# Performance work log

Hardware: AMD Instinct MI355X
Metric: run time of the kernel (lower is better)

Reference implementation:

```python
import jax, jax.numpy as jnp
import numpy as np

B, H, S, D = 2, 16, 2048, 64
DEGREE = 2
EPS = 1e-4


def setup_inputs() -> dict:
    key = jax.random.key(0)
    kq, kk, kv = jax.random.split(key, 3)
    q = jax.random.normal(kq, (B, H, S, D), dtype=jnp.float32)
    k = jax.random.normal(kk, (B, H, S, D), dtype=jnp.float32)
    v = jax.random.normal(kv, (B, H, S, D), dtype=jnp.float32)
    return {"q": q, "k": k, "v": v}


def reference(q, k, v):
    # dots: [B,H,S,S] = QK^T
    dots = jnp.einsum("bhsd,bhtd->bhst", q, k)
    # polynomial kernel: x^degree, row-normalized with clamped denom
    x = dots ** DEGREE
    denom = jnp.maximum(x.sum(axis=-1, keepdims=True), EPS)
    attn = x / denom
    # weighted V sum: [B,H,S,D]
    return jnp.einsum("bhst,bhtd->bhsd", attn, v)
```

## Files before the change

kernel.cpp:

```cpp
#include <hip/hip_runtime.h>


#define S_LEN 2048
#define DH    64
#define BQ    128
#define BK    64
#define LSTR  72
#define EPSTR 68
#define PSTR  65
#define BH_N  32
#define PER_BH (S_LEN * DH)
#define NT    (S_LEN / BK)

typedef __bf16 bf16x8 __attribute__((ext_vector_type(8)));
typedef __bf16 bf16x2 __attribute__((ext_vector_type(2)));
typedef float  f32x4  __attribute__((ext_vector_type(4)));
typedef float  f32x16 __attribute__((ext_vector_type(16)));
typedef unsigned int uivec2 __attribute__((ext_vector_type(2)));

__device__ __forceinline__ unsigned short f2bf(float f) {
    union { float f; unsigned int u; } x; x.f = f;
    unsigned int u = x.u;
    return (unsigned short)((u + 0x7fffu + ((u >> 16) & 1u)) >> 16);
}

__device__ __forceinline__ unsigned int pack2bf(float lo, float hi) {
#if __has_builtin(__builtin_amdgcn_cvt_pk_bf16_f32)
    bf16x2 p = __builtin_amdgcn_cvt_pk_bf16_f32(lo, hi);
    union { bf16x2 v; unsigned int u; } c; c.v = p;
    return c.u;
#else
    return (unsigned int)f2bf(lo) | ((unsigned int)f2bf(hi) << 16);
#endif
}

__device__ __forceinline__ void pl32swap(unsigned int& a, unsigned int& b) {
#if __has_builtin(__builtin_amdgcn_permlane32_swap)
    uivec2 r = __builtin_amdgcn_permlane32_swap(a, b, false, false);
    a = r[0]; b = r[1];
#else
    asm("v_permlane32_swap_b32 %0, %1" : "+v"(a), "+v"(b));
#endif
}

__global__ __launch_bounds__(256)
void prepass_kernel(const float* __restrict__ kg, const float* __restrict__ vg,
                    unsigned short* __restrict__ kbf, unsigned short* __restrict__ vt)
{
    __shared__ unsigned short Ls[64 * PSTR];
    const int tid = threadIdx.x;
    const int bh  = blockIdx.y;
    const int t0  = blockIdx.x * 64;
    const size_t base = (size_t)bh * PER_BH + (size_t)t0 * DH;

    {
        const float4* src = (const float4*)(kg + base + (size_t)tid * 16);
        float4 a = src[0], b = src[1], c = src[2], d = src[3];
        union { unsigned short h[8]; uint4 v; } u0, u1;
        u0.h[0]=f2bf(a.x); u0.h[1]=f2bf(a.y); u0.h[2]=f2bf(a.z); u0.h[3]=f2bf(a.w);
        u0.h[4]=f2bf(b.x); u0.h[5]=f2bf(b.y); u0.h[6]=f2bf(b.z); u0.h[7]=f2bf(b.w);
        u1.h[0]=f2bf(c.x); u1.h[1]=f2bf(c.y); u1.h[2]=f2bf(c.z); u1.h[3]=f2bf(c.w);
        u1.h[4]=f2bf(d.x); u1.h[5]=f2bf(d.y); u1.h[6]=f2bf(d.z); u1.h[7]=f2bf(d.w);
        uint4* dst = (uint4*)(kbf + base + (size_t)tid * 16);
        dst[0] = u0.v; dst[1] = u1.v;
    }

    const float* vb = vg + base;
    #pragma unroll
    for (int r = 0; r < 4; ++r) {
        int idx = r * 256 + tid;
        int row = idx >> 4, c4 = idx & 15;
        float4 f = ((const float4*)vb)[idx];
        unsigned short* p = &Ls[row * PSTR + c4 * 4];
        p[0] = f2bf(f.x); p[1] = f2bf(f.y); p[2] = f2bf(f.z); p[3] = f2bf(f.w);
    }
    __syncthreads();
    #pragma unroll
    for (int r = 0; r < 2; ++r) {
        int idx = r * 256 + tid;
        int d = idx >> 3, j8 = idx & 7;
        union { unsigned short h[8]; uint4 v; } u;
        #pragma unroll
        for (int jj = 0; jj < 8; ++jj) u.h[jj] = Ls[(j8 * 8 + jj) * PSTR + d];
        *(uint4*)(vt + (size_t)bh * PER_BH + (size_t)d * S_LEN + t0 + j8 * 8) = u.v;
    }
}

__global__ __launch_bounds__(256, 2)
void poly_attn_main(const float* __restrict__ qg,
                    const unsigned short* __restrict__ kbf,
                    const unsigned short* __restrict__ vtbf,
                    float* __restrict__ og)
{
    __shared__ __align__(16) unsigned short smem[4 * 64 * LSTR];
    #define KS_BASE(b)  ((b) * 64 * LSTR)
    #define VTS_BASE(b) ((2 + (b)) * 64 * LSTR)

    const int tid  = threadIdx.x;
    const int lane = tid & 63;
    const int w    = tid >> 6;
    const int l31  = lane & 31;
    const int h    = lane >> 5;

    const int bh = blockIdx.y;
    const int q0 = blockIdx.x * BQ;

    const float* qb = qg + ((size_t)bh * S_LEN + q0) * DH;
    const unsigned short* kb  = kbf  + (size_t)bh * PER_BH;
    const unsigned short* vtb = vtbf + (size_t)bh * PER_BH;
    float* ob = og + ((size_t)bh * S_LEN + q0) * DH;

    bf16x8 qfrag[4];
    #pragma unroll
    for (int ks = 0; ks < 4; ++ks) {
        const float* qp = qb + (32 * w + l31) * DH + ks * 16 + h * 8;
        float4 f0 = *(const float4*)qp;
        float4 f1 = *(const float4*)(qp + 4);
        union { unsigned int d[4]; bf16x8 v; } u;
        u.d[0] = pack2bf(f0.x, f0.y);
        u.d[1] = pack2bf(f0.z, f0.w);
        u.d[2] = pack2bf(f1.x, f1.y);
        u.d[3] = pack2bf(f1.z, f1.w);
        qfrag[ks] = u.v;
    }

    f32x16 oacc[2];
    #pragma unroll
    for (int mt = 0; mt < 2; ++mt)
        #pragma unroll
        for (int r = 0; r < 16; ++r) oacc[mt][r] = 0.f;
    float dsum = 0.f;

    const int srow = tid >> 3;
    const int sc8  = tid & 7;

    uint4 kreg[2], vreg[2];
    #pragma unroll
    for (int it = 0; it < 2; ++it) {
        int row = srow + it * 32;
        kreg[it] = *(const uint4*)(kb + (size_t)row * DH + sc8 * 8);
        vreg[it] = *(const uint4*)(vtb + (size_t)row * S_LEN + sc8 * 8);
    }
    #pragma unroll
    for (int it = 0; it < 2; ++it) {
        int row = srow + it * 32;
        *(uint4*)&smem[KS_BASE(0)  + row * LSTR + sc8 * 8] = kreg[it];
        *(uint4*)&smem[VTS_BASE(0) + row * LSTR + sc8 * 8] = vreg[it];
    }
    __syncthreads();

    for (int t = 0; t < NT; ++t) {
        const int cur = t & 1;
        if (t + 1 < NT) {
            const int t0n = (t + 1) * BK;
            #pragma unroll
            for (int it = 0; it < 2; ++it) {
                int row = srow + it * 32;
                kreg[it] = *(const uint4*)(kb + (size_t)(t0n + row) * DH + sc8 * 8);
                vreg[it] = *(const uint4*)(vtb + (size_t)row * S_LEN + t0n + sc8 * 8);
            }
        }

        unsigned int bfrag[4][4];
        #pragma unroll
        for (int jt = 0; jt < 2; ++jt) {
            f32x16 acc;
            #pragma unroll
            for (int r = 0; r < 16; ++r) acc[r] = 0.f;
            #pragma unroll
            for (int ks = 0; ks < 4; ++ks) {
                bf16x8 kf = *(const bf16x8*)&smem[KS_BASE(cur) + (jt * 32 + l31) * LSTR + ks * 16 + h * 8];
                acc = __builtin_amdgcn_mfma_f32_32x32x16_bf16(kf, qfrag[ks], acc, 0, 0, 0);
            }
            unsigned int pk[4][2];
            #pragma unroll
            for (int g = 0; g < 4; ++g) {
                float x0 = acc[4*g+0], x1 = acc[4*g+1], x2 = acc[4*g+2], x3 = acc[4*g+3];
                x0 *= x0; x1 *= x1; x2 *= x2; x3 *= x3;
                dsum += (x0 + x1) + (x2 + x3);
                pk[g][0] = pack2bf(x0, x1);
                pk[g][1] = pack2bf(x2, x3);
            }
            #pragma unroll
            for (int e = 0; e < 2; ++e) {
                unsigned int a0 = pk[2*e][0], b0 = pk[2*e+1][0];
                unsigned int a1 = pk[2*e][1], b1 = pk[2*e+1][1];
                pl32swap(a0, b0);
                pl32swap(a1, b1);
                const int ks = jt * 2 + e;
                bfrag[ks][0] = a0; bfrag[ks][1] = a1;
                bfrag[ks][2] = b0; bfrag[ks][3] = b1;
            }
        }

        #pragma unroll
        for (int mt = 0; mt < 2; ++mt) {
            #pragma unroll
            for (int ks = 0; ks < 4; ++ks) {
                bf16x8 vf = *(const bf16x8*)&smem[VTS_BASE(cur) + (mt * 32 + l31) * LSTR + ks * 16 + h * 8];
                union { unsigned int d[4]; bf16x8 v; } u;
                u.d[0] = bfrag[ks][0]; u.d[1] = bfrag[ks][1];
                u.d[2] = bfrag[ks][2]; u.d[3] = bfrag[ks][3];
                oacc[mt] = __builtin_amdgcn_mfma_f32_32x32x16_bf16(vf, u.v, oacc[mt], 0, 0, 0);
            }
        }

        if (t + 1 < NT) {
            #pragma unroll
            for (int it = 0; it < 2; ++it) {
                int row = srow + it * 32;
                *(uint4*)&smem[KS_BASE(cur ^ 1)  + row * LSTR + sc8 * 8] = kreg[it];
                *(uint4*)&smem[VTS_BASE(cur ^ 1) + row * LSTR + sc8 * 8] = vreg[it];
            }
            __syncthreads();
        }
    }

    float tot = dsum + __shfl_xor(dsum, 32);
    float inv = 1.0f / fmaxf(tot, 1e-4f);

    __syncthreads();
    float* ep = (float*)smem + (size_t)w * (32 * EPSTR);
    #pragma unroll
    for (int mt = 0; mt < 2; ++mt) {
        #pragma unroll
        for (int g = 0; g < 4; ++g) {
            f32x4 vv;
            vv[0] = oacc[mt][4*g+0] * inv;
            vv[1] = oacc[mt][4*g+1] * inv;
            vv[2] = oacc[mt][4*g+2] * inv;
            vv[3] = oacc[mt][4*g+3] * inv;
            *(f32x4*)&ep[l31 * EPSTR + mt * 32 + 8 * g + 4 * h] = vv;
        }
    }
    const int quad4 = lane >> 4;
    const int c4    = lane & 15;
    #pragma unroll
    for (int rr = 0; rr < 8; ++rr) {
        int row = rr * 4 + quad4;
        f32x4 vv = *(const f32x4*)&ep[row * EPSTR + c4 * 4];
        *(f32x4*)&ob[(32 * w + row) * DH + c4 * 4] = vv;
    }
    #undef KS_BASE
    #undef VTS_BASE
}

__global__ __launch_bounds__(256, 2)
void poly_attn_fallback(const float* __restrict__ qg, const float* __restrict__ kg,
                        const float* __restrict__ vg, float* __restrict__ og)
{
    __shared__ unsigned short Qs[64 * LSTR];
    __shared__ unsigned short Ksl[64 * LSTR];
    __shared__ unsigned short Vt[64 * LSTR];
    __shared__ unsigned short Xsl[64 * LSTR];

    const int tid  = threadIdx.x;
    const int lane = tid & 63;
    const int w    = tid >> 6;
    const int c    = lane & 15;
    const int quad = lane >> 4;
    const int i0   = w * 16;

    const int bh = blockIdx.y;
    const int q0 = blockIdx.x * 64;

    const float* qb = qg + ((size_t)bh * S_LEN + q0) * DH;
    const float* kb = kg + (size_t)bh * S_LEN * DH;
    const float* vb = vg + (size_t)bh * S_LEN * DH;
    float*       ob = og + ((size_t)bh * S_LEN + q0) * DH;

    {
        const float4* qf4 = (const float4*)qb;
        #pragma unroll
        for (int r = 0; r < 4; ++r) {
            int idx = r * 256 + tid;
            int row = idx >> 4, c4 = idx & 15;
            float4 f = qf4[idx];
            ushort4 hh;
            hh.x = f2bf(f.x); hh.y = f2bf(f.y); hh.z = f2bf(f.z); hh.w = f2bf(f.w);
            *(ushort4*)&Qs[row * LSTR + c4 * 4] = hh;
        }
    }

    f32x4 oacc[4];
    #pragma unroll
    for (int t = 0; t < 4; ++t) { oacc[t][0]=0.f; oacc[t][1]=0.f; oacc[t][2]=0.f; oacc[t][3]=0.f; }
    float dsum[4] = {0.f, 0.f, 0.f, 0.f};

    for (int t0 = 0; t0 < S_LEN; t0 += 64) {
        __syncthreads();
        {
            const float4* kf4 = (const float4*)(kb + (size_t)t0 * DH);
            const float4* vf4 = (const float4*)(vb + (size_t)t0 * DH);
            #pragma unroll
            for (int r = 0; r < 4; ++r) {
                int idx = r * 256 + tid;
                int row = idx >> 4, c4 = idx & 15;
                float4 f = kf4[idx];
                ushort4 hh;
                hh.x = f2bf(f.x); hh.y = f2bf(f.y); hh.z = f2bf(f.z); hh.w = f2bf(f.w);
                *(ushort4*)&Ksl[row * LSTR + c4 * 4] = hh;
                float4 g = vf4[idx];
                int d0 = c4 * 4;
                Vt[(d0 + 0) * LSTR + row] = f2bf(g.x);
                Vt[(d0 + 1) * LSTR + row] = f2bf(g.y);
                Vt[(d0 + 2) * LSTR + row] = f2bf(g.z);
                Vt[(d0 + 3) * LSTR + row] = f2bf(g.w);
            }
        }
        __syncthreads();

        f32x4 xacc[4];
        #pragma unroll
        for (int t = 0; t < 4; ++t) { xacc[t][0]=0.f; xacc[t][1]=0.f; xacc[t][2]=0.f; xacc[t][3]=0.f; }
        #pragma unroll
        for (int k0 = 0; k0 < 64; k0 += 32) {
            bf16x8 af = *(const bf16x8*)&Qs[(i0 + c) * LSTR + k0 + quad * 8];
            #pragma unroll
            for (int tn = 0; tn < 4; ++tn) {
                bf16x8 bfg = *(const bf16x8*)&Ksl[(tn * 16 + c) * LSTR + k0 + quad * 8];
                xacc[tn] = __builtin_amdgcn_mfma_f32_16x16x32_bf16(af, bfg, xacc[tn], 0, 0, 0);
            }
        }
        #pragma unroll
        for (int tn = 0; tn < 4; ++tn)
            #pragma unroll
            for (int r = 0; r < 4; ++r) {
                float xv = xacc[tn][r];
                float xs = xv * xv;
                dsum[r] += xs;
                Xsl[(i0 + quad * 4 + r) * LSTR + tn * 16 + c] = f2bf(xs);
            }
        __syncthreads();

        #pragma unroll
        for (int k0 = 0; k0 < 64; k0 += 32) {
            bf16x8 af = *(const bf16x8*)&Xsl[(i0 + c) * LSTR + k0 + quad * 8];
            #pragma unroll
            for (int tn = 0; tn < 4; ++tn) {
                bf16x8 bfg = *(const bf16x8*)&Vt[(tn * 16 + c) * LSTR + k0 + quad * 8];
                oacc[tn] = __builtin_amdgcn_mfma_f32_16x16x32_bf16(af, bfg, oacc[tn], 0, 0, 0);
            }
        }
    }

    #pragma unroll
    for (int r = 0; r < 4; ++r) {
        float s = dsum[r];
        s += __shfl_xor(s, 1);
        s += __shfl_xor(s, 2);
        s += __shfl_xor(s, 4);
        s += __shfl_xor(s, 8);
        dsum[r] = 1.0f / fmaxf(s, 1e-4f);
    }
    #pragma unroll
    for (int tn = 0; tn < 4; ++tn)
        #pragma unroll
        for (int r = 0; r < 4; ++r)
            ob[(i0 + quad * 4 + r) * DH + tn * 16 + c] = oacc[tn][r] * dsum[r];
}

extern "C" void kernel_launch(void* const* d_in, const int* in_sizes, int n_in,
                              void* d_out, int out_size, void* d_ws, size_t ws_size,
                              hipStream_t stream) {
    (void)in_sizes; (void)n_in; (void)out_size;
    const float* q = (const float*)d_in[0];
    const float* k = (const float*)d_in[1];
    const float* v = (const float*)d_in[2];
    float* o = (float*)d_out;

    const size_t elems = (size_t)BH_N * PER_BH;
    const size_t need  = 2 * elems * sizeof(unsigned short);

    if (ws_size >= need) {
        unsigned short* kbf = (unsigned short*)d_ws;
        unsigned short* vtb = kbf + elems;
        prepass_kernel<<<dim3(S_LEN / 64, BH_N), 256, 0, stream>>>(k, v, kbf, vtb);
        poly_attn_main<<<dim3(S_LEN / BQ, BH_N), 256, 0, stream>>>(q, kbf, vtb, o);
    } else {
        poly_attn_fallback<<<dim3(S_LEN / 64, BH_N), 256, 0, stream>>>(q, k, v, o);
    }
}
```

Measured before the change: 159.2 us.

## Halve query tile and split key block across wave pairs with smem reduction

Query tile per block drops from 128 to 64 rows, and each pair of waves now shares 32 query rows, with each wave handling half of every 64-key tile. Partial outputs and row denominators are combined through shared memory in the epilogue. Launch bounds are raised to 4 blocks per SM. This doubles the grid and cuts per-wave MFMA work per tile to improve occupancy and latency hiding, at the cost of twice the K/V tile loads per query and an extra cross-wave reduction.

```diff
diff --git a/kernel.cpp b/kernel.cpp
--- a/kernel.cpp
+++ b/kernel.cpp
@@ -3,7 +3,7 @@
 
 #define S_LEN 2048
 #define DH    64
-#define BQ    128
+#define BQ    64
 #define BK    64
 #define LSTR  72
 #define EPSTR 68
@@ -86,19 +86,22 @@
     }
 }
 
-__global__ __launch_bounds__(256, 2)
+__global__ __launch_bounds__(256, 4)
 void poly_attn_main(const float* __restrict__ qg,
                     const unsigned short* __restrict__ kbf,
                     const unsigned short* __restrict__ vtbf,
                     float* __restrict__ og)
 {
     __shared__ __align__(16) unsigned short smem[4 * 64 * LSTR];
+    __shared__ float dbuf[128];
     #define KS_BASE(b)  ((b) * 64 * LSTR)
     #define VTS_BASE(b) ((2 + (b)) * 64 * LSTR)
 
     const int tid  = threadIdx.x;
     const int lane = tid & 63;
     const int w    = tid >> 6;
+    const int p    = w >> 1;
+    const int e    = w & 1;
     const int l31  = lane & 31;
     const int h    = lane >> 5;
 
@@ -113,7 +116,7 @@
     bf16x8 qfrag[4];
     #pragma unroll
     for (int ks = 0; ks < 4; ++ks) {
-        const float* qp = qb + (32 * w + l31) * DH + ks * 16 + h * 8;
+        const float* qp = qb + (32 * p + l31) * DH + ks * 16 + h * 8;
         float4 f0 = *(const float4*)qp;
         float4 f1 = *(const float4*)(qp + 4);
         union { unsigned int d[4]; bf16x8 v; } u;
@@ -161,46 +164,43 @@
             }
         }
 
-        unsigned int bfrag[4][4];
-        #pragma unroll
-        for (int jt = 0; jt < 2; ++jt) {
-            f32x16 acc;
-            #pragma unroll
-            for (int r = 0; r < 16; ++r) acc[r] = 0.f;
-            #pragma unroll
-            for (int ks = 0; ks < 4; ++ks) {
-                bf16x8 kf = *(const bf16x8*)&smem[KS_BASE(cur) + (jt * 32 + l31) * LSTR + ks * 16 + h * 8];
-                acc = __builtin_amdgcn_mfma_f32_32x32x16_bf16(kf, qfrag[ks], acc, 0, 0, 0);
-            }
-            unsigned int pk[4][2];
-            #pragma unroll
-            for (int g = 0; g < 4; ++g) {
-                float x0 = acc[4*g+0], x1 = acc[4*g+1], x2 = acc[4*g+2], x3 = acc[4*g+3];
-                x0 *= x0; x1 *= x1; x2 *= x2; x3 *= x3;
-                dsum += (x0 + x1) + (x2 + x3);
-                pk[g][0] = pack2bf(x0, x1);
-                pk[g][1] = pack2bf(x2, x3);
-            }
-            #pragma unroll
-            for (int e = 0; e < 2; ++e) {
-                unsigned int a0 = pk[2*e][0], b0 = pk[2*e+1][0];
-                unsigned int a1 = pk[2*e][1], b1 = pk[2*e+1][1];
-                pl32swap(a0, b0);
-                pl32swap(a1, b1);
-                const int ks = jt * 2 + e;
-                bfrag[ks][0] = a0; bfrag[ks][1] = a1;
-                bfrag[ks][2] = b0; bfrag[ks][3] = b1;
-            }
+        f32x16 acc;
+        #pragma unroll
+        for (int r = 0; r < 16; ++r) acc[r] = 0.f;
+        #pragma unroll
+        for (int ks = 0; ks < 4; ++ks) {
+            bf16x8 kf = *(const bf16x8*)&smem[KS_BASE(cur) + (e * 32 + l31) * LSTR + ks * 16 + h * 8];
+            acc = __builtin_amdgcn_mfma_f32_32x32x16_bf16(kf, qfrag[ks], acc, 0, 0, 0);
+        }
+
+        unsigned int pk[4][2];
+        #pragma unroll
+        for (int g = 0; g < 4; ++g) {
+            float x0 = acc[4*g+0], x1 = acc[4*g+1], x2 = acc[4*g+2], x3 = acc[4*g+3];
+            x0 *= x0; x1 *= x1; x2 *= x2; x3 *= x3;
+            dsum += (x0 + x1) + (x2 + x3);
+            pk[g][0] = pack2bf(x0, x1);
+            pk[g][1] = pack2bf(x2, x3);
+        }
+        unsigned int bfrag[2][4];
+        #pragma unroll
+        for (int ksl = 0; ksl < 2; ++ksl) {
+            unsigned int a0 = pk[2*ksl][0], b0 = pk[2*ksl+1][0];
+            unsigned int a1 = pk[2*ksl][1], b1 = pk[2*ksl+1][1];
+            pl32swap(a0, b0);
+            pl32swap(a1, b1);
+            bfrag[ksl][0] = a0; bfrag[ksl][1] = a1;
+            bfrag[ksl][2] = b0; bfrag[ksl][3] = b1;
         }
 
         #pragma unroll
         for (int mt = 0; mt < 2; ++mt) {
             #pragma unroll
-            for (int ks = 0; ks < 4; ++ks) {
-                bf16x8 vf = *(const bf16x8*)&smem[VTS_BASE(cur) + (mt * 32 + l31) * LSTR + ks * 16 + h * 8];
+            for (int ksl = 0; ksl < 2; ++ksl) {
+                bf16x8 vf = *(const bf16x8*)&smem[VTS_BASE(cur) + (mt * 32 + l31) * LSTR + e * 32 + ksl * 16 + h * 8];
                 union { unsigned int d[4]; bf16x8 v; } u;
-                u.d[0] = bfrag[ks][0]; u.d[1] = bfrag[ks][1];
-                u.d[2] = bfrag[ks][2]; u.d[3] = bfrag[ks][3];
+                u.d[0] = bfrag[ksl][0]; u.d[1] = bfrag[ksl][1];
+                u.d[2] = bfrag[ksl][2]; u.d[3] = bfrag[ksl][3];
                 oacc[mt] = __builtin_amdgcn_mfma_f32_32x32x16_bf16(vf, u.v, oacc[mt], 0, 0, 0);
             }
         }
@@ -216,8 +216,7 @@
         }
     }
 
-    float tot = dsum + __shfl_xor(dsum, 32);
-    float inv = 1.0f / fmaxf(tot, 1e-4f);
+    float wavetot = dsum + __shfl_xor(dsum, 32);
 
     __syncthreads();
     float* ep = (float*)smem + (size_t)w * (32 * EPSTR);
@@ -226,20 +225,32 @@
         #pragma unroll
         for (int g = 0; g < 4; ++g) {
             f32x4 vv;
-            vv[0] = oacc[mt][4*g+0] * inv;
-            vv[1] = oacc[mt][4*g+1] * inv;
-            vv[2] = oacc[mt][4*g+2] * inv;
-            vv[3] = oacc[mt][4*g+3] * inv;
+            vv[0] = oacc[mt][4*g+0];
+            vv[1] = oacc[mt][4*g+1];
+            vv[2] = oacc[mt][4*g+2];
+            vv[3] = oacc[mt][4*g+3];
             *(f32x4*)&ep[l31 * EPSTR + mt * 32 + 8 * g + 4 * h] = vv;
         }
     }
-    const int quad4 = lane >> 4;
-    const int c4    = lane & 15;
-    #pragma unroll
-    for (int rr = 0; rr < 8; ++rr) {
-        int row = rr * 4 + quad4;
-        f32x4 vv = *(const f32x4*)&ep[row * EPSTR + c4 * 4];
-        *(f32x4*)&ob[(32 * w + row) * DH + c4 * 4] = vv;
+    if (h == 0) dbuf[w * 32 + l31] = wavetot;
+    __syncthreads();
+
+    const float* ep0 = (float*)smem + (size_t)(2 * p)     * (32 * EPSTR);
+    const float* ep1 = (float*)smem + (size_t)(2 * p + 1) * (32 * EPSTR);
+    const int lrow = e * 16 + (lane >> 2);
+    const float den = dbuf[2 * p * 32 + lrow] + dbuf[(2 * p + 1) * 32 + lrow];
+    const float inv = 1.0f / fmaxf(den, 1e-4f);
+    #pragma unroll
+    for (int it = 0; it < 4; ++it) {
+        int d0 = (lane & 3) * 16 + it * 4;
+        f32x4 a = *(const f32x4*)&ep0[lrow * EPSTR + d0];
+        f32x4 b = *(const f32x4*)&ep1[lrow * EPSTR + d0];
+        f32x4 s;
+        s[0] = (a[0] + b[0]) * inv;
+        s[1] = (a[1] + b[1]) * inv;
+        s[2] = (a[2] + b[2]) * inv;
+        s[3] = (a[3] + b[3]) * inv;
+        *(f32x4*)&ob[(32 * p + lrow) * DH + d0] = s;
     }
     #undef KS_BASE
     #undef VTS_BASE
```

Measured after the change: 155.5 us. 1.02x faster.
